# Performance work log

Measured on AMD Instinct MI355X. Metric: run time of the kernel, lower is better.

The kernel has to match this reference:

```python
import jax, jax.numpy as jnp
import numpy as np

N_NODES = 100000


def _gcn_norm(edge_index, num_nodes):
    # PyG GCNConv default: add self-loops, symmetric normalization.
    src, dst = edge_index[0], edge_index[1]
    loop = jnp.arange(num_nodes, dtype=src.dtype)
    src = jnp.concatenate([src, loop])
    dst = jnp.concatenate([dst, loop])
    deg = jax.ops.segment_sum(jnp.ones_like(dst, dtype=jnp.float32), dst,
                              num_segments=num_nodes)
    dinv = jnp.where(deg > 0, jax.lax.rsqrt(jnp.maximum(deg, 1.0)), 0.0)
    norm = dinv[src] * dinv[dst]  # [E + N]
    return src, dst, norm


def _gcn_layer(x, src, dst, norm, W, b, num_nodes):
    h = x @ W                              # [N, out]
    msg = h[src] * norm[:, None]           # gather + scale, [E+N, out]
    agg = jax.ops.segment_sum(msg, dst, num_segments=num_nodes)  # scatter-add
    return agg + b


def setup_inputs() -> dict:
    key = jax.random.key(0)
    ks = jax.random.split(key, 12)
    in_c, hid = 64, 128
    dims = [in_c, hid, hid // 2, hid // 4, hid // 8, 1]
    x = jax.random.normal(ks[0], (N_NODES, in_c), dtype=jnp.float32)
    edge_index = jax.random.randint(ks[1], (2, 1600000), 0, N_NODES,
                                    dtype=jnp.int64)
    inp = {"x": x, "edge_index": edge_index}
    for i in range(5):
        fan_in = dims[i]
        s = 1.0 / np.sqrt(fan_in)
        inp[f"W{i+1}"] = jax.random.uniform(ks[2 + 2 * i], (dims[i], dims[i + 1]),
                                            minval=-s, maxval=s,
                                            dtype=jnp.float32)
        inp[f"b{i+1}"] = jnp.zeros((dims[i + 1],), dtype=jnp.float32)
    return inp


def reference(x, edge_index, W1, b1, W2, b2, W3, b3, W4, b4, W5, b5):
    num_nodes = x.shape[0]
    src, dst, norm = _gcn_norm(edge_index, num_nodes)
    h = _gcn_layer(x, src, dst, norm, W1, b1, num_nodes)
    h = jax.nn.relu(h)
    h = _gcn_layer(h, src, dst, norm, W2, b2, num_nodes)
    h = jax.nn.relu(h)
    h = _gcn_layer(h, src, dst, norm, W3, b3, num_nodes)
    h = jax.nn.relu(h)
    h = _gcn_layer(h, src, dst, norm, W4, b4, num_nodes)
    h = jax.nn.relu(h)
    h = _gcn_layer(h, src, dst, norm, W5, b5, num_nodes)
    return h
```

## Files before the change

### kernel.cpp

```cpp
#include <hip/hip_runtime.h>
#include <math.h>


#define NBIN_MAX 256
#define BSHIFT 9
#define BINW 512
#define CHUNK 8192

__global__ __launch_bounds__(256) void k_hist(const int* __restrict__ dst, int E,
                                              int nbin, int* __restrict__ binCnt) {
    __shared__ int h[NBIN_MAX];
    int t = threadIdx.x;
    for (int i = t; i < nbin; i += 256) h[i] = 0;
    __syncthreads();
    for (int e = blockIdx.x * 256 + t; e < E; e += gridDim.x * 256)
        atomicAdd(&h[dst[e] >> BSHIFT], 1);
    __syncthreads();
    for (int i = t; i < nbin; i += 256)
        if (h[i]) atomicAdd(&binCnt[i], h[i]);
}

__global__ __launch_bounds__(256) void k_binscan(const int* __restrict__ binCnt,
                                                 int nbin, int* __restrict__ binBase,
                                                 int* __restrict__ binCur) {
    __shared__ int sh[256];
    int t = threadIdx.x;
    int v = (t < nbin) ? binCnt[t] : 0;
    sh[t] = v;
    __syncthreads();
    for (int d = 1; d < 256; d <<= 1) {
        int u = (t >= d) ? sh[t - d] : 0;
        __syncthreads();
        sh[t] += u;
        __syncthreads();
    }
    int ex = sh[t] - v;
    if (t < nbin) { binBase[t] = ex; binCur[t] = ex; }
    if (t == nbin - 1) binBase[nbin] = sh[t];
}

__global__ __launch_bounds__(256) void k_binfill(const int* __restrict__ src,
                                                 const int* __restrict__ dst, int E,
                                                 int nbin, int* __restrict__ binCur,
                                                 unsigned* __restrict__ tmp) {
    __shared__ int h[NBIN_MAX];
    __shared__ int res[NBIN_MAX];
    int t = threadIdx.x;
    int e0 = blockIdx.x * CHUNK;
    int e1 = min(e0 + CHUNK, E);
    for (int i = t; i < nbin; i += 256) h[i] = 0;
    __syncthreads();
    for (int e = e0 + t; e < e1; e += 256)
        atomicAdd(&h[dst[e] >> BSHIFT], 1);
    __syncthreads();
    for (int i = t; i < nbin; i += 256)
        res[i] = h[i] ? atomicAdd(&binCur[i], h[i]) : 0;
    __syncthreads();
    for (int i = t; i < nbin; i += 256) h[i] = 0;
    __syncthreads();
    for (int e = e0 + t; e < e1; e += 256) {
        int d = dst[e];
        int b = d >> BSHIFT;
        int p = res[b] + atomicAdd(&h[b], 1);
        tmp[p] = ((unsigned)src[e] << BSHIFT) | (unsigned)(d & (BINW - 1));
    }
}

__global__ __launch_bounds__(256) void k_csr(const unsigned* __restrict__ tmp,
                                             const int* __restrict__ binBase,
                                             int n, int nbin,
                                             float* __restrict__ dinv,
                                             int* __restrict__ offs,
                                             int* __restrict__ csr) {
    __shared__ int ldeg[BINW];
    __shared__ int loff[BINW];
    __shared__ int pair[256];
    int b = blockIdx.x;
    int t = threadIdx.x;
    ldeg[t] = 0; ldeg[t + 256] = 0;
    __syncthreads();
    int lo = binBase[b], hi = binBase[b + 1];
    for (int p = lo + t; p < hi; p += 256)
        atomicAdd(&ldeg[tmp[p] & (BINW - 1u)], 1);
    __syncthreads();
    int a0 = ldeg[2 * t], a1 = ldeg[2 * t + 1];
    pair[t] = a0 + a1;
    __syncthreads();
    int v = pair[t];
    for (int d = 1; d < 256; d <<= 1) {
        int u = (t >= d) ? pair[t - d] : 0;
        __syncthreads();
        pair[t] += u;
        __syncthreads();
    }
    int ex = pair[t] - v;
    loff[2 * t] = ex;
    loff[2 * t + 1] = ex + a0;
    __syncthreads();
    int v0 = b << BSHIFT;
    for (int i = t; i < BINW; i += 256) {
        int vv = v0 + i;
        if (vv < n) {
            offs[vv] = lo + loff[i];
            dinv[vv] = 1.0f / sqrtf((float)(ldeg[i] + 1));
        }
    }
    if (t == 0 && b == nbin - 1) offs[n] = hi;
    __syncthreads();
    ldeg[t] = 0; ldeg[t + 256] = 0;
    __syncthreads();
    for (int p = lo + t; p < hi; p += 256) {
        unsigned u = tmp[p];
        int d0 = (int)(u & (BINW - 1u));
        int pos = loff[d0] + atomicAdd(&ldeg[d0], 1);
        csr[lo + pos] = (int)(u >> BSHIFT);
    }
}

template <int W, bool RELU, bool BIAS, bool L1SCALE>
__global__ __launch_bounds__(256) void k_aggv(const float* __restrict__ S,
                                              const float* __restrict__ dinv,
                                              const int* __restrict__ offs,
                                              const int* __restrict__ csr,
                                              const float* __restrict__ bg,
                                              float* __restrict__ Y, int n) {
    constexpr int LPR = W / 4;
    constexpr int G = 64 / LPR;
    int lane = threadIdx.x & 63;
    int wave = threadIdx.x >> 6;
    int v = blockIdx.x * 4 + wave;
    if (v >= n) return;
    int g = lane / LPR;
    int j = lane % LPR;
    float dv = dinv[v];
    float4 acc0 = make_float4(0.f, 0.f, 0.f, 0.f);
    float4 acc1 = make_float4(0.f, 0.f, 0.f, 0.f);
    if (g == 0) {
        float4 xv = *(const float4*)&S[(size_t)v * W + j * 4];
        float sc = L1SCALE ? dv : 1.0f;
        acc0.x = xv.x * sc; acc0.y = xv.y * sc; acc0.z = xv.z * sc; acc0.w = xv.w * sc;
    }
    int e0 = offs[v], re = offs[v + 1];
    for (int eb = e0; eb < re; eb += 2 * G) {
        int ea = eb + g, ec = eb + G + g;
        if (ea < re) {
            int u = csr[ea];
            float4 a = *(const float4*)&S[(size_t)u * W + j * 4];
            float sc = L1SCALE ? dinv[u] : 1.0f;
            acc0.x += a.x * sc; acc0.y += a.y * sc; acc0.z += a.z * sc; acc0.w += a.w * sc;
        }
        if (ec < re) {
            int u = csr[ec];
            float4 a = *(const float4*)&S[(size_t)u * W + j * 4];
            float sc = L1SCALE ? dinv[u] : 1.0f;
            acc1.x += a.x * sc; acc1.y += a.y * sc; acc1.z += a.z * sc; acc1.w += a.w * sc;
        }
    }
    acc0.x += acc1.x; acc0.y += acc1.y; acc0.z += acc1.z; acc0.w += acc1.w;
#pragma unroll
    for (int d = LPR; d < 64; d <<= 1) {
        acc0.x += __shfl_xor(acc0.x, d);
        acc0.y += __shfl_xor(acc0.y, d);
        acc0.z += __shfl_xor(acc0.z, d);
        acc0.w += __shfl_xor(acc0.w, d);
    }
    if (lane < LPR) {
        float4 r;
        r.x = dv * acc0.x; r.y = dv * acc0.y; r.z = dv * acc0.z; r.w = dv * acc0.w;
        if (BIAS) {
            float4 bv = *(const float4*)&bg[j * 4];
            r.x += bv.x; r.y += bv.y; r.z += bv.z; r.w += bv.w;
        }
        if (RELU) {
            r.x = fmaxf(r.x, 0.f); r.y = fmaxf(r.y, 0.f);
            r.z = fmaxf(r.z, 0.f); r.w = fmaxf(r.w, 0.f);
        }
        *(float4*)&Y[(size_t)v * W + j * 4] = r;
    }
}

__global__ __launch_bounds__(256) void k_agg16_gemm5(const float* __restrict__ S,
                                                     const float* __restrict__ dinv,
                                                     const int* __restrict__ offs,
                                                     const int* __restrict__ csr,
                                                     const float* __restrict__ b4,
                                                     const float* __restrict__ W5,
                                                     float* __restrict__ Y, int n) {
    constexpr int W = 16, LPR = 4, G = 16;
    int lane = threadIdx.x & 63;
    int wave = threadIdx.x >> 6;
    int v = blockIdx.x * 4 + wave;
    if (v >= n) return;
    int g = lane / LPR;
    int j = lane % LPR;
    float dv = dinv[v];
    float4 acc0 = make_float4(0.f, 0.f, 0.f, 0.f);
    float4 acc1 = make_float4(0.f, 0.f, 0.f, 0.f);
    if (g == 0) acc0 = *(const float4*)&S[(size_t)v * W + j * 4];
    int e0 = offs[v], re = offs[v + 1];
    for (int eb = e0; eb < re; eb += 2 * G) {
        int ea = eb + g, ec = eb + G + g;
        if (ea < re) {
            int u = csr[ea];
            float4 a = *(const float4*)&S[(size_t)u * W + j * 4];
            acc0.x += a.x; acc0.y += a.y; acc0.z += a.z; acc0.w += a.w;
        }
        if (ec < re) {
            int u = csr[ec];
            float4 a = *(const float4*)&S[(size_t)u * W + j * 4];
            acc1.x += a.x; acc1.y += a.y; acc1.z += a.z; acc1.w += a.w;
        }
    }
    acc0.x += acc1.x; acc0.y += acc1.y; acc0.z += acc1.z; acc0.w += acc1.w;
#pragma unroll
    for (int d = LPR; d < 64; d <<= 1) {
        acc0.x += __shfl_xor(acc0.x, d);
        acc0.y += __shfl_xor(acc0.y, d);
        acc0.z += __shfl_xor(acc0.z, d);
        acc0.w += __shfl_xor(acc0.w, d);
    }
    float4 bv = *(const float4*)&b4[j * 4];
    float4 w5 = *(const float4*)&W5[j * 4];
    float hx = fmaxf(dv * acc0.x + bv.x, 0.f);
    float hy = fmaxf(dv * acc0.y + bv.y, 0.f);
    float hz = fmaxf(dv * acc0.z + bv.z, 0.f);
    float hw = fmaxf(dv * acc0.w + bv.w, 0.f);
    float p = hx * w5.x + hy * w5.y + hz * w5.z + hw * w5.w;
    p += __shfl_xor(p, 1);
    p += __shfl_xor(p, 2);
    if (lane == 0) Y[v] = p * dv;
}

__global__ __launch_bounds__(256) void k_agg1(const float* __restrict__ S,
                                              const float* __restrict__ dinv,
                                              const int* __restrict__ offs,
                                              const int* __restrict__ csr,
                                              const float* __restrict__ bg,
                                              float* __restrict__ Y, int n) {
    int v = blockIdx.x * 256 + threadIdx.x;
    if (v >= n) return;
    float sum = S[v];
    int e = offs[v], re = offs[v + 1];
    for (; e < re; ++e) sum += S[csr[e]];
    Y[v] = dinv[v] * sum + bg[0];
}

template <int IN, int OUT, int EPI>
__global__ __launch_bounds__(256) void k_gemm(const float* __restrict__ X,
                                              const float* __restrict__ Wg,
                                              const float* __restrict__ bg,
                                              const float* __restrict__ dinv,
                                              float* __restrict__ Y, int nrows) {
    constexpr int TPR = OUT / 4;
    constexpr int GROUPS = 256 / TPR;
    constexpr int ROWS = GROUPS * 2;
    __shared__ __align__(16) float Wl[IN * OUT];
    __shared__ __align__(16) float xl[ROWS * IN];
    __shared__ float bl[OUT];
    int tid = threadIdx.x;
    for (int i = tid; i < IN * OUT; i += 256) Wl[i] = Wg[i];
    if (EPI == 0)
        for (int i = tid; i < OUT; i += 256) bl[i] = bg[i];
    int base = blockIdx.x * ROWS;
    for (int i = tid; i < ROWS * IN; i += 256) {
        int r = base + i / IN;
        xl[i] = (r < nrows) ? X[(size_t)base * IN + i] : 0.0f;
    }
    __syncthreads();
    int g = tid / TPR;
    int c0 = (tid % TPR) * 4;
    int r0 = base + g * 2, r1 = r0 + 1;
    int l0 = (g * 2) * IN, l1 = l0 + IN;
    float4 acc0 = make_float4(0.f, 0.f, 0.f, 0.f);
    float4 acc1 = make_float4(0.f, 0.f, 0.f, 0.f);
#pragma unroll 8
    for (int k = 0; k < IN; ++k) {
        float4 w = *(const float4*)&Wl[k * OUT + c0];
        float a0 = xl[l0 + k], a1 = xl[l1 + k];
        acc0.x += a0 * w.x; acc0.y += a0 * w.y; acc0.z += a0 * w.z; acc0.w += a0 * w.w;
        acc1.x += a1 * w.x; acc1.y += a1 * w.y; acc1.z += a1 * w.z; acc1.w += a1 * w.w;
    }
    if (EPI == 0) {
        float bx = bl[c0], by = bl[c0 + 1], bz = bl[c0 + 2], bw = bl[c0 + 3];
        acc0.x = fmaxf(acc0.x + bx, 0.f); acc0.y = fmaxf(acc0.y + by, 0.f);
        acc0.z = fmaxf(acc0.z + bz, 0.f); acc0.w = fmaxf(acc0.w + bw, 0.f);
        acc1.x = fmaxf(acc1.x + bx, 0.f); acc1.y = fmaxf(acc1.y + by, 0.f);
        acc1.z = fmaxf(acc1.z + bz, 0.f); acc1.w = fmaxf(acc1.w + bw, 0.f);
    } else {
        if (r0 < nrows) { float d0 = dinv[r0]; acc0.x *= d0; acc0.y *= d0; acc0.z *= d0; acc0.w *= d0; }
        if (r1 < nrows) { float d1 = dinv[r1]; acc1.x *= d1; acc1.y *= d1; acc1.z *= d1; acc1.w *= d1; }
    }
    if (r0 < nrows) *(float4*)&Y[(size_t)r0 * OUT + c0] = acc0;
    if (r1 < nrows) *(float4*)&Y[(size_t)r1 * OUT + c0] = acc1;
}

extern "C" void kernel_launch(void* const* d_in, const int* in_sizes, int n_in,
                              void* d_out, int out_size, void* d_ws, size_t ws_size,
                              hipStream_t stream) {
    const float* x  = (const float*)d_in[0];
    const int*   ei = (const int*)d_in[1];
    const float* W1 = (const float*)d_in[2];  const float* b1 = (const float*)d_in[3];
    const float* W2 = (const float*)d_in[4];  const float* b2 = (const float*)d_in[5];
    const float* W3 = (const float*)d_in[6];  const float* b3 = (const float*)d_in[7];
    const float* W4 = (const float*)d_in[8];  const float* b4 = (const float*)d_in[9];
    const float* W5 = (const float*)d_in[10]; const float* b5 = (const float*)d_in[11];

    const int N = in_sizes[0] / 64;
    const int E = in_sizes[1] / 2;
    const int* src = ei;
    const int* dst = ei + E;
    const int nbin = (N + BINW - 1) / BINW;

    char* ws = (char*)d_ws;
    size_t off = 0;
    auto alloc = [&](size_t bytes) -> void* {
        void* p = ws + off;
        off = (off + bytes + 255) & ~(size_t)255;
        return p;
    };
    float* dinv    = (float*)alloc((size_t)N * 4);
    int*   offs    = (int*)alloc((size_t)(N + 1) * 4);
    int*   binCnt  = (int*)alloc((size_t)NBIN_MAX * 4);
    int*   binBase = (int*)alloc((size_t)(NBIN_MAX + 1) * 4);
    int*   binCur  = (int*)alloc((size_t)NBIN_MAX * 4);
    int*   csr     = (int*)alloc((size_t)E * 4);
    float* s5      = (float*)alloc((size_t)N * 4);
    float* A       = (float*)alloc((size_t)N * 128 * 4);
    float* B       = (float*)alloc((size_t)N * 64 * 4);
    float* C       = (float*)alloc((size_t)N * 64 * 4);
    unsigned* tmp  = (unsigned*)C;

    hipMemsetAsync(binCnt, 0, (size_t)NBIN_MAX * 4, stream);

    k_hist<<<256, 256, 0, stream>>>(dst, E, nbin, binCnt);
    k_binscan<<<1, 256, 0, stream>>>(binCnt, nbin, binBase, binCur);
    k_binfill<<<(E + CHUNK - 1) / CHUNK, 256, 0, stream>>>(src, dst, E, nbin, binCur, tmp);
    k_csr<<<nbin, 256, 0, stream>>>(tmp, binBase, N, nbin, dinv, offs, csr);

    const int gagg = (N + 3) / 4;
    k_aggv<64, false, false, true><<<gagg, 256, 0, stream>>>(x, dinv, offs, csr, nullptr, B, N);
    k_gemm<64, 128, 0><<<(N + 15) / 16, 256, 0, stream>>>(B, W1, b1, nullptr, A, N);
    k_gemm<128, 64, 1><<<(N + 31) / 32, 256, 0, stream>>>(A, W2, nullptr, dinv, B, N);
    k_aggv<64, true, true, false><<<gagg, 256, 0, stream>>>(B, dinv, offs, csr, b2, C, N);
    k_gemm<64, 32, 1><<<(N + 63) / 64, 256, 0, stream>>>(C, W3, nullptr, dinv, B, N);
    k_aggv<32, true, true, false><<<gagg, 256, 0, stream>>>(B, dinv, offs, csr, b3, A, N);
    k_gemm<32, 16, 1><<<(N + 127) / 128, 256, 0, stream>>>(A, W4, nullptr, dinv, B, N);
    k_agg16_gemm5<<<gagg, 256, 0, stream>>>(B, dinv, offs, csr, b4, W5, s5, N);
    k_agg1<<<(N + 255) / 256, 256, 0, stream>>>(s5, dinv, offs, csr, b5, (float*)d_out, N);
}
```

Baseline: 424.8 us.

## Slice feature matrices into 8-column planes for cache-friendly gather aggregation

Feature matrices feeding the aggregation are stored column-sliced: each 8-float slice of all nodes is laid out contiguously, and the GEMM epilogues write that layout directly. A new pre-scaling kernel handles layer 1 by pre-multiplying x by dinv. Each aggregation block then processes one slice for 16 nodes, so the gathered working set per slice (N*32 bytes) is far more likely to stay resident in L2/MALL during random neighbor gathers. In exchange the CSR indices are read once per slice, using nontemporal loads, and an extra pass over x is added.

```diff
diff --git a/kernel.cpp b/kernel.cpp
--- a/kernel.cpp
+++ b/kernel.cpp
@@ -117,65 +117,78 @@
     }
 }
 
-template <int W, bool RELU, bool BIAS, bool L1SCALE>
-__global__ __launch_bounds__(256) void k_aggv(const float* __restrict__ S,
+__global__ __launch_bounds__(256) void k_slice(const float* __restrict__ x,
+                                               const float* __restrict__ dinv,
+                                               float* __restrict__ xs, int n) {
+    int i = blockIdx.x * 256 + threadIdx.x;
+    int v = i >> 4;
+    if (v >= n) return;
+    int c4 = i & 15;
+    float4 a = *(const float4*)&x[(size_t)v * 64 + c4 * 4];
+    float dv = dinv[v];
+    a.x *= dv; a.y *= dv; a.z *= dv; a.w *= dv;
+    int slice = c4 >> 1, j = c4 & 1;
+    *(float4*)&xs[(size_t)slice * n * 8 + (size_t)v * 8 + j * 4] = a;
+}
+
+template <int W, int SLICES, bool RELU, bool BIAS>
+__global__ __launch_bounds__(256) void k_aggs(const float* __restrict__ S,
                                               const float* __restrict__ dinv,
                                               const int* __restrict__ offs,
                                               const int* __restrict__ csr,
                                               const float* __restrict__ bg,
                                               float* __restrict__ Y, int n) {
-    constexpr int LPR = W / 4;
-    constexpr int G = 64 / LPR;
     int lane = threadIdx.x & 63;
     int wave = threadIdx.x >> 6;
-    int v = blockIdx.x * 4 + wave;
-    if (v >= n) return;
-    int g = lane / LPR;
-    int j = lane % LPR;
-    float dv = dinv[v];
+    int slice = blockIdx.x % SLICES;
+    int vb = (blockIdx.x / SLICES) * 16 + wave * 4;
+    int rg = lane >> 4;
+    int l16 = lane & 15;
+    int g = l16 >> 1;
+    int j = l16 & 1;
+    int v = vb + rg;
+    bool act = v < n;
+    const float* Sb = S + (size_t)slice * n * 8;
+    float dv = act ? dinv[v] : 0.f;
     float4 acc0 = make_float4(0.f, 0.f, 0.f, 0.f);
     float4 acc1 = make_float4(0.f, 0.f, 0.f, 0.f);
-    if (g == 0) {
-        float4 xv = *(const float4*)&S[(size_t)v * W + j * 4];
-        float sc = L1SCALE ? dv : 1.0f;
-        acc0.x = xv.x * sc; acc0.y = xv.y * sc; acc0.z = xv.z * sc; acc0.w = xv.w * sc;
-    }
-    int e0 = offs[v], re = offs[v + 1];
-    for (int eb = e0; eb < re; eb += 2 * G) {
-        int ea = eb + g, ec = eb + G + g;
+    int e0 = 0, re = 0;
+    if (act) { e0 = offs[v]; re = offs[v + 1]; }
+    if (act && g == 0)
+        acc0 = *(const float4*)&Sb[(size_t)v * 8 + j * 4];
+    for (int eb = e0; eb < re; eb += 16) {
+        int ea = eb + g, ec = eb + 8 + g;
         if (ea < re) {
-            int u = csr[ea];
-            float4 a = *(const float4*)&S[(size_t)u * W + j * 4];
-            float sc = L1SCALE ? dinv[u] : 1.0f;
-            acc0.x += a.x * sc; acc0.y += a.y * sc; acc0.z += a.z * sc; acc0.w += a.w * sc;
+            int u = __builtin_nontemporal_load(&csr[ea]);
+            float4 a = *(const float4*)&Sb[(size_t)u * 8 + j * 4];
+            acc0.x += a.x; acc0.y += a.y; acc0.z += a.z; acc0.w += a.w;
         }
         if (ec < re) {
-            int u = csr[ec];
-            float4 a = *(const float4*)&S[(size_t)u * W + j * 4];
-            float sc = L1SCALE ? dinv[u] : 1.0f;
-            acc1.x += a.x * sc; acc1.y += a.y * sc; acc1.z += a.z * sc; acc1.w += a.w * sc;
+            int u = __builtin_nontemporal_load(&csr[ec]);
+            float4 a = *(const float4*)&Sb[(size_t)u * 8 + j * 4];
+            acc1.x += a.x; acc1.y += a.y; acc1.z += a.z; acc1.w += a.w;
         }
     }
     acc0.x += acc1.x; acc0.y += acc1.y; acc0.z += acc1.z; acc0.w += acc1.w;
 #pragma unroll
-    for (int d = LPR; d < 64; d <<= 1) {
+    for (int d = 2; d < 16; d <<= 1) {
         acc0.x += __shfl_xor(acc0.x, d);
         acc0.y += __shfl_xor(acc0.y, d);
         acc0.z += __shfl_xor(acc0.z, d);
         acc0.w += __shfl_xor(acc0.w, d);
     }
-    if (lane < LPR) {
+    if (act && l16 < 2) {
         float4 r;
         r.x = dv * acc0.x; r.y = dv * acc0.y; r.z = dv * acc0.z; r.w = dv * acc0.w;
         if (BIAS) {
-            float4 bv = *(const float4*)&bg[j * 4];
+            float4 bv = *(const float4*)&bg[slice * 8 + j * 4];
             r.x += bv.x; r.y += bv.y; r.z += bv.z; r.w += bv.w;
         }
         if (RELU) {
             r.x = fmaxf(r.x, 0.f); r.y = fmaxf(r.y, 0.f);
             r.z = fmaxf(r.z, 0.f); r.w = fmaxf(r.w, 0.f);
         }
-        *(float4*)&Y[(size_t)v * W + j * 4] = r;
+        *(float4*)&Y[(size_t)v * W + slice * 8 + j * 4] = r;
     }
 }
 
@@ -245,7 +258,7 @@
     Y[v] = dinv[v] * sum + bg[0];
 }
 
-template <int IN, int OUT, int EPI>
+template <int IN, int OUT, int EPI, int OSL>
 __global__ __launch_bounds__(256) void k_gemm(const float* __restrict__ X,
                                               const float* __restrict__ Wg,
                                               const float* __restrict__ bg,
@@ -286,12 +299,20 @@
         acc0.z = fmaxf(acc0.z + bz, 0.f); acc0.w = fmaxf(acc0.w + bw, 0.f);
         acc1.x = fmaxf(acc1.x + bx, 0.f); acc1.y = fmaxf(acc1.y + by, 0.f);
         acc1.z = fmaxf(acc1.z + bz, 0.f); acc1.w = fmaxf(acc1.w + bw, 0.f);
+        if (r0 < nrows) *(float4*)&Y[(size_t)r0 * OUT + c0] = acc0;
+        if (r1 < nrows) *(float4*)&Y[(size_t)r1 * OUT + c0] = acc1;
     } else {
         if (r0 < nrows) { float d0 = dinv[r0]; acc0.x *= d0; acc0.y *= d0; acc0.z *= d0; acc0.w *= d0; }
         if (r1 < nrows) { float d1 = dinv[r1]; acc1.x *= d1; acc1.y *= d1; acc1.z *= d1; acc1.w *= d1; }
-    }
-    if (r0 < nrows) *(float4*)&Y[(size_t)r0 * OUT + c0] = acc0;
-    if (r1 < nrows) *(float4*)&Y[(size_t)r1 * OUT + c0] = acc1;
+        if (OSL > 0) {
+            size_t sa = (size_t)(c0 >> 3) * nrows * 8 + (size_t)r0 * 8 + (c0 & 7);
+            if (r0 < nrows) *(float4*)&Y[sa] = acc0;
+            if (r1 < nrows) *(float4*)&Y[sa + 8] = acc1;
+        } else {
+            if (r0 < nrows) *(float4*)&Y[(size_t)r0 * OUT + c0] = acc0;
+            if (r1 < nrows) *(float4*)&Y[(size_t)r1 * OUT + c0] = acc1;
+        }
+    }
 }
 
 extern "C" void kernel_launch(void* const* d_in, const int* in_sizes, int n_in,
@@ -329,6 +350,7 @@
     float* B       = (float*)alloc((size_t)N * 64 * 4);
     float* C       = (float*)alloc((size_t)N * 64 * 4);
     unsigned* tmp  = (unsigned*)C;
+    float* xs      = A;
 
     hipMemsetAsync(binCnt, 0, (size_t)NBIN_MAX * 4, stream);
 
@@ -337,14 +359,15 @@
     k_binfill<<<(E + CHUNK - 1) / CHUNK, 256, 0, stream>>>(src, dst, E, nbin, binCur, tmp);
     k_csr<<<nbin, 256, 0, stream>>>(tmp, binBase, N, nbin, dinv, offs, csr);
 
-    const int gagg = (N + 3) / 4;
-    k_aggv<64, false, false, true><<<gagg, 256, 0, stream>>>(x, dinv, offs, csr, nullptr, B, N);
-    k_gemm<64, 128, 0><<<(N + 15) / 16, 256, 0, stream>>>(B, W1, b1, nullptr, A, N);
-    k_gemm<128, 64, 1><<<(N + 31) / 32, 256, 0, stream>>>(A, W2, nullptr, dinv, B, N);
-    k_aggv<64, true, true, false><<<gagg, 256, 0, stream>>>(B, dinv, offs, csr, b2, C, N);
-    k_gemm<64, 32, 1><<<(N + 63) / 64, 256, 0, stream>>>(C, W3, nullptr, dinv, B, N);
-    k_aggv<32, true, true, false><<<gagg, 256, 0, stream>>>(B, dinv, offs, csr, b3, A, N);
-    k_gemm<32, 16, 1><<<(N + 127) / 128, 256, 0, stream>>>(A, W4, nullptr, dinv, B, N);
-    k_agg16_gemm5<<<gagg, 256, 0, stream>>>(B, dinv, offs, csr, b4, W5, s5, N);
+    const int grow = (N + 15) / 16;
+    k_slice<<<(N * 16 + 255) / 256, 256, 0, stream>>>(x, dinv, xs, N);
+    k_aggs<64, 8, false, false><<<grow * 8, 256, 0, stream>>>(xs, dinv, offs, csr, nullptr, B, N);
+    k_gemm<64, 128, 0, 0><<<(N + 15) / 16, 256, 0, stream>>>(B, W1, b1, nullptr, A, N);
+    k_gemm<128, 64, 1, 8><<<(N + 31) / 32, 256, 0, stream>>>(A, W2, nullptr, dinv, B, N);
+    k_aggs<64, 8, true, true><<<grow * 8, 256, 0, stream>>>(B, dinv, offs, csr, b2, C, N);
+    k_gemm<64, 32, 1, 4><<<(N + 63) / 64, 256, 0, stream>>>(C, W3, nullptr, dinv, B, N);
+    k_aggs<32, 4, true, true><<<grow * 4, 256, 0, stream>>>(B, dinv, offs, csr, b3, A, N);
+    k_gemm<32, 16, 1, 0><<<(N + 127) / 128, 256, 0, stream>>>(A, W4, nullptr, dinv, B, N);
+    k_agg16_gemm5<<<(N + 3) / 4, 256, 0, stream>>>(B, dinv, offs, csr, b4, W5, s5, N);
     k_agg1<<<(N + 255) / 256, 256, 0, stream>>>(s5, dinv, offs, csr, b5, (float*)d_out, N);
 }
```

After: 602.6 us. +41.9%, slower.
